# Performance work log

Measured on AMD Instinct MI355X. Metric: run time of the kernel, lower is better.

## Reference

```python
import jax, jax.numpy as jnp
import numpy as np

N_NODES = 50000
N_EDGES = 500000
D = 256  # node_dim = edge_dim = out_dim; in_dim = 2*D


def setup_inputs() -> dict:
    key = jax.random.key(0)
    ks = jax.random.split(key, 9)
    x = jax.random.normal(ks[0], (N_NODES, D), dtype=jnp.float32)
    edge_index = jax.random.randint(ks[1], (2, N_EDGES), 0, N_NODES, dtype=jnp.int64)
    edge_attr = jax.random.normal(ks[2], (N_EDGES, D), dtype=jnp.float32)
    u = jax.random.normal(ks[3], (1, D), dtype=jnp.float32)
    batch = jnp.zeros((N_NODES,), dtype=jnp.int64)
    scale = 1.0 / np.sqrt(2 * D)
    W1 = jax.random.normal(ks[4], (2 * D, D), dtype=jnp.float32) * scale
    b1 = jax.random.normal(ks[5], (D,), dtype=jnp.float32) * scale
    W2 = jax.random.normal(ks[6], (2 * D, D), dtype=jnp.float32) * scale
    b2 = jax.random.normal(ks[7], (D,), dtype=jnp.float32) * scale
    return {"x": x, "edge_index": edge_index, "edge_attr": edge_attr, "u": u,
            "batch": batch, "W1": W1, "b1": b1, "W2": W2, "b2": b2}


def reference(x, edge_index, edge_attr, u, batch, W1, b1, W2, b2):
    row, col = edge_index[0], edge_index[1]
    # gather source-node features and concat with edge features: [E, 2D]
    h = jnp.concatenate([x[row], edge_attr], axis=1)
    h = jax.nn.relu(h @ W1 + b1)  # node_mlp_1
    # scatter-mean over destination nodes
    agg = jax.ops.segment_sum(h, col, num_segments=N_NODES)
    cnt = jax.ops.segment_sum(jnp.ones((h.shape[0],), h.dtype), col, num_segments=N_NODES)
    agg = agg / jnp.maximum(cnt, 1.0)[:, None]
    out = jnp.concatenate([x, agg], axis=1)  # [N, 2D]
    return jax.nn.relu(out @ W2 + b2)  # node_mlp_2
```

## Files before the change

### kernel.cpp

```cpp
#include <hip/hip_runtime.h>

#define N_NODES 50000
#define N_EDGES 500000
#define D 256
#define TWO_D 512

typedef __attribute__((ext_vector_type(8))) __bf16 bf16x8;
typedef __attribute__((ext_vector_type(4))) float f32x4;
typedef unsigned short ushort_t;

__device__ __forceinline__ unsigned short f2bf(float f) {
    unsigned int u = __builtin_bit_cast(unsigned int, f);
    u += 0x7FFFu + ((u >> 16) & 1u);
    return (unsigned short)(u >> 16);
}
__device__ __forceinline__ unsigned int pk2(float lo, float hi) {
    return (unsigned int)f2bf(lo) | ((unsigned int)f2bf(hi) << 16);
}
__device__ __forceinline__ float bf2f(ushort_t u) {
    return __builtin_bit_cast(float, ((unsigned int)u) << 16);
}


__global__ void k_zero(float* __restrict__ p, int n4) {
    int i = blockIdx.x * blockDim.x + threadIdx.x;
    if (i < n4) ((float4*)p)[i] = make_float4(0.f, 0.f, 0.f, 0.f);
}

__global__ void k_cvt_x(const float* __restrict__ x, ushort_t* __restrict__ xb, int n8) {
    int i = blockIdx.x * blockDim.x + threadIdx.x;
    if (i < n8) {
        const float4* s = (const float4*)(x + (size_t)i * 8);
        float4 a = s[0], b = s[1];
        uint4 o;
        o.x = pk2(a.x, a.y); o.y = pk2(a.z, a.w);
        o.z = pk2(b.x, b.y); o.w = pk2(b.z, b.w);
        *(uint4*)(xb + (size_t)i * 8) = o;
    }
}

__global__ void k_wt(const float* __restrict__ w, ushort_t* __restrict__ wt) {
    int n = blockIdx.x;
    for (int k = threadIdx.x; k < TWO_D; k += blockDim.x)
        wt[(size_t)n * TWO_D + k] = f2bf(w[(size_t)k * D + n]);
}

__global__ void k_count_i(const int* __restrict__ coli, int* __restrict__ cnt) {
    int e = blockIdx.x * blockDim.x + threadIdx.x;
    if (e < N_EDGES) atomicAdd(&cnt[coli[e]], 1);
}

__global__ void k_count_f(const int* __restrict__ coli, float* __restrict__ cnt) {
    int e = blockIdx.x * blockDim.x + threadIdx.x;
    if (e < N_EDGES) atomicAdd(&cnt[coli[e]], 1.0f);
}


__device__ __forceinline__ int iscan_block(int v, int tid) {
    int lane = tid & 63, wv = tid >> 6;
    int s = v;
    #pragma unroll
    for (int off = 1; off < 64; off <<= 1) {
        int t = __shfl_up(s, off, 64);
        if (lane >= off) s += t;
    }
    __shared__ int wsum[4];
    if (lane == 63) wsum[wv] = s;
    __syncthreads();
    #pragma unroll
    for (int w = 0; w < 3; ++w)
        if (wv > w) s += wsum[w];
    return s;
}

__global__ void k_scan_a(const int* __restrict__ cnt, int* __restrict__ rowptr,
                         int* __restrict__ bsum) {
    int i = blockIdx.x * 256 + threadIdx.x;
    int v = (i < N_NODES) ? cnt[i] : 0;
    int s = iscan_block(v, threadIdx.x);
    if (i < N_NODES) rowptr[i] = s - v;
    if (threadIdx.x == 255) bsum[blockIdx.x] = s;
}

__global__ void k_scan_b(int* __restrict__ bsum, int nb) {
    int i = threadIdx.x;
    int v = (i < nb) ? bsum[i] : 0;
    int s = iscan_block(v, i);
    if (i < nb) bsum[i] = s - v;
}

__global__ void k_scan_c(int* __restrict__ rowptr, const int* __restrict__ bsum,
                         int* __restrict__ cursor) {
    int i = blockIdx.x * 256 + threadIdx.x;
    if (i < N_NODES) {
        int r = rowptr[i] + bsum[blockIdx.x];
        rowptr[i] = r;
        cursor[i] = r;
    }
    if (i == 0) rowptr[N_NODES] = N_EDGES;
}

__global__ void k_fill(const int* __restrict__ coli, int* __restrict__ cursor,
                       int* __restrict__ elist) {
    int e = blockIdx.x * blockDim.x + threadIdx.x;
    if (e < N_EDGES) {
        int p = atomicAdd(&cursor[coli[e]], 1);
        elist[p] = e;
    }
}

template<bool CSR>
__global__ __launch_bounds__(256) void k_edge_t(
    const ushort_t* __restrict__ xb, const float* __restrict__ ea,
    const ushort_t* __restrict__ w1t, const float* __restrict__ b1,
    const int* __restrict__ rowi, const int* __restrict__ coli,
    ushort_t* __restrict__ h, float* __restrict__ agg)
{
    __shared__ __align__(16) ushort_t As[64 * 64];
    __shared__ __align__(16) ushort_t Bs[256 * 64];
    const int tid = threadIdx.x;
    const int wave = tid >> 6, lane = tid & 63;
    const int lr = lane & 15, lh = lane >> 4;
    const int e0 = blockIdx.x * 64;

    const int sm = tid >> 2;
    const int sc = (tid & 3) << 4;
    int es = e0 + sm; if (es >= N_EDGES) es = N_EDGES - 1;
    const int srow = rowi[es];
    const ushort_t* xrow  = xb + (size_t)srow * D;
    const float*    earow = ea + (size_t)es * D;
    const ushort_t* wrow  = w1t + (size_t)tid * TWO_D;
    const int swA = (sm & 7) << 3;
    const int swB = (tid & 7) << 3;

    f32x4 acc[4][4];
    #pragma unroll
    for (int i = 0; i < 4; ++i)
        #pragma unroll
        for (int j = 0; j < 4; ++j)
            acc[i][j] = (f32x4){0.f, 0.f, 0.f, 0.f};

    for (int kk = 0; kk < 8; ++kk) {
        const int k0 = kk << 6;
        uint4 av0, av1;
        if (kk < 4) {
            const uint4* s = (const uint4*)(xrow + k0 + sc);
            av0 = s[0]; av1 = s[1];
        } else {
            const float4* s = (const float4*)(earow + (k0 - D) + sc);
            float4 f0 = s[0], f1 = s[1], f2 = s[2], f3 = s[3];
            av0.x = pk2(f0.x, f0.y); av0.y = pk2(f0.z, f0.w);
            av0.z = pk2(f1.x, f1.y); av0.w = pk2(f1.z, f1.w);
            av1.x = pk2(f2.x, f2.y); av1.y = pk2(f2.z, f2.w);
            av1.z = pk2(f3.x, f3.y); av1.w = pk2(f3.z, f3.w);
        }
        const uint4* wsv = (const uint4*)(wrow + k0);
        uint4 w0 = wsv[0], w1 = wsv[1], w2 = wsv[2], w3 = wsv[3];
        uint4 w4 = wsv[4], w5 = wsv[5], w6 = wsv[6], w7 = wsv[7];

        __syncthreads();
        *(uint4*)&As[sm * 64 + ( sc      ^ swA)] = av0;
        *(uint4*)&As[sm * 64 + ((sc + 8) ^ swA)] = av1;
        {
            const int base = tid * 64;
            *(uint4*)&Bs[base + ( 0 ^ swB)] = w0;
            *(uint4*)&Bs[base + ( 8 ^ swB)] = w1;
            *(uint4*)&Bs[base + (16 ^ swB)] = w2;
            *(uint4*)&Bs[base + (24 ^ swB)] = w3;
            *(uint4*)&Bs[base + (32 ^ swB)] = w4;
            *(uint4*)&Bs[base + (40 ^ swB)] = w5;
            *(uint4*)&Bs[base + (48 ^ swB)] = w6;
            *(uint4*)&Bs[base + (56 ^ swB)] = w7;
        }
        __syncthreads();

        #pragma unroll
        for (int kh = 0; kh < 2; ++kh) {
            const int kb = kh * 32 + lh * 8;
            bf16x8 af[4], bfr[4];
            #pragma unroll
            for (int i = 0; i < 4; ++i) {
                int m = i * 16 + lr;
                af[i] = *(const bf16x8*)&As[m * 64 + (kb ^ ((m & 7) << 3))];
            }
            #pragma unroll
            for (int j = 0; j < 4; ++j) {
                int n = wave * 64 + j * 16 + lr;
                bfr[j] = *(const bf16x8*)&Bs[n * 64 + (kb ^ ((n & 7) << 3))];
            }
            #pragma unroll
            for (int i = 0; i < 4; ++i)
                #pragma unroll
                for (int j = 0; j < 4; ++j)
                    acc[i][j] = __builtin_amdgcn_mfma_f32_16x16x32_bf16(af[i], bfr[j], acc[i][j], 0, 0, 0);
        }
    }

    float bv[4];
    #pragma unroll
    for (int j = 0; j < 4; ++j) bv[j] = b1[wave * 64 + j * 16 + lr];
    #pragma unroll
    for (int i = 0; i < 4; ++i) {
        #pragma unroll
        for (int r = 0; r < 4; ++r) {
            int m = i * 16 + lh * 4 + r;
            int e = e0 + m;
            if (e < N_EDGES) {
                if constexpr (CSR) {
                    ushort_t* hrow = h + (size_t)e * D + wave * 64 + lr;
                    #pragma unroll
                    for (int j = 0; j < 4; ++j) {
                        float v = acc[i][j][r] + bv[j];
                        hrow[j * 16] = f2bf(v > 0.f ? v : 0.f);
                    }
                } else {
                    float* arow = agg + (size_t)coli[e] * D;
                    #pragma unroll
                    for (int j = 0; j < 4; ++j) {
                        float v = acc[i][j][r] + bv[j];
                        if (v > 0.f) atomicAdd(&arow[wave * 64 + j * 16 + lr], v);
                    }
                }
            }
        }
    }
}

__global__ __launch_bounds__(256) void k_agg(
    const ushort_t* __restrict__ h, const int* __restrict__ rowptr,
    const int* __restrict__ elist, ushort_t* __restrict__ aggb)
{
    int node = blockIdx.x * 4 + (threadIdx.x >> 6);
    if (node >= N_NODES) return;
    int lane = threadIdx.x & 63;
    int beg = rowptr[node], end = rowptr[node + 1];
    float a0 = 0.f, a1 = 0.f, a2 = 0.f, a3 = 0.f;
    int p = beg;
    int e_nxt = (p < end) ? elist[p] : 0;
    while (p < end) {
        int e = e_nxt;
        if (p + 1 < end) e_nxt = elist[p + 1];
        ushort4 u = *(const ushort4*)(h + (size_t)e * D + lane * 4);
        a0 += bf2f(u.x); a1 += bf2f(u.y); a2 += bf2f(u.z); a3 += bf2f(u.w);
        ++p;
    }
    float inv = 1.0f / fmaxf((float)(end - beg), 1.0f);
    ushort4 o;
    o.x = f2bf(a0 * inv); o.y = f2bf(a1 * inv);
    o.z = f2bf(a2 * inv); o.w = f2bf(a3 * inv);
    *(ushort4*)(aggb + (size_t)node * D + lane * 4) = o;
}

template<bool CSR>
__global__ __launch_bounds__(256) void k_node_t(
    const ushort_t* __restrict__ xb, const ushort_t* __restrict__ aggb,
    const float* __restrict__ aggf, const float* __restrict__ cnt,
    const ushort_t* __restrict__ w2t, const float* __restrict__ b2,
    float* __restrict__ out)
{
    __shared__ __align__(16) ushort_t As[64 * 64];
    __shared__ __align__(16) ushort_t Bs[256 * 64];
    const int tid = threadIdx.x;
    const int wave = tid >> 6, lane = tid & 63;
    const int lr = lane & 15, lh = lane >> 4;
    const int n0 = blockIdx.x * 64;

    const int sm = tid >> 2;
    const int sc = (tid & 3) << 4;
    int ns = n0 + sm; if (ns >= N_NODES) ns = N_NODES - 1;
    const ushort_t* xrow = xb + (size_t)ns * D;
    const ushort_t* abrow = CSR ? (aggb + (size_t)ns * D) : nullptr;
    const float*    afrow = CSR ? nullptr : (aggf + (size_t)ns * D);
    const float     ic    = CSR ? 1.0f : (1.0f / fmaxf(cnt[ns], 1.0f));
    const ushort_t* wrow = w2t + (size_t)tid * TWO_D;
    const int swA = (sm & 7) << 3;
    const int swB = (tid & 7) << 3;

    f32x4 acc[4][4];
    #pragma unroll
    for (int i = 0; i < 4; ++i)
        #pragma unroll
        for (int j = 0; j < 4; ++j)
            acc[i][j] = (f32x4){0.f, 0.f, 0.f, 0.f};

    for (int kk = 0; kk < 8; ++kk) {
        const int k0 = kk << 6;
        uint4 av0, av1;
        if (kk < 4) {
            const uint4* s = (const uint4*)(xrow + k0 + sc);
            av0 = s[0]; av1 = s[1];
        } else if constexpr (CSR) {
            const uint4* s = (const uint4*)(abrow + (k0 - D) + sc);
            av0 = s[0]; av1 = s[1];
        } else {
            const float4* s = (const float4*)(afrow + (k0 - D) + sc);
            float4 f0 = s[0], f1 = s[1], f2 = s[2], f3 = s[3];
            f0.x *= ic; f0.y *= ic; f0.z *= ic; f0.w *= ic;
            f1.x *= ic; f1.y *= ic; f1.z *= ic; f1.w *= ic;
            f2.x *= ic; f2.y *= ic; f2.z *= ic; f2.w *= ic;
            f3.x *= ic; f3.y *= ic; f3.z *= ic; f3.w *= ic;
            av0.x = pk2(f0.x, f0.y); av0.y = pk2(f0.z, f0.w);
            av0.z = pk2(f1.x, f1.y); av0.w = pk2(f1.z, f1.w);
            av1.x = pk2(f2.x, f2.y); av1.y = pk2(f2.z, f2.w);
            av1.z = pk2(f3.x, f3.y); av1.w = pk2(f3.z, f3.w);
        }
        const uint4* wsv = (const uint4*)(wrow + k0);
        uint4 w0 = wsv[0], w1 = wsv[1], w2 = wsv[2], w3 = wsv[3];
        uint4 w4 = wsv[4], w5 = wsv[5], w6 = wsv[6], w7 = wsv[7];

        __syncthreads();
        *(uint4*)&As[sm * 64 + ( sc      ^ swA)] = av0;
        *(uint4*)&As[sm * 64 + ((sc + 8) ^ swA)] = av1;
        {
            const int base = tid * 64;
            *(uint4*)&Bs[base + ( 0 ^ swB)] = w0;
            *(uint4*)&Bs[base + ( 8 ^ swB)] = w1;
            *(uint4*)&Bs[base + (16 ^ swB)] = w2;
            *(uint4*)&Bs[base + (24 ^ swB)] = w3;
            *(uint4*)&Bs[base + (32 ^ swB)] = w4;
            *(uint4*)&Bs[base + (40 ^ swB)] = w5;
            *(uint4*)&Bs[base + (48 ^ swB)] = w6;
            *(uint4*)&Bs[base + (56 ^ swB)] = w7;
        }
        __syncthreads();

        #pragma unroll
        for (int kh = 0; kh < 2; ++kh) {
            const int kb = kh * 32 + lh * 8;
            bf16x8 af[4], bfr[4];
            #pragma unroll
            for (int i = 0; i < 4; ++i) {
                int m = i * 16 + lr;
                af[i] = *(const bf16x8*)&As[m * 64 + (kb ^ ((m & 7) << 3))];
            }
            #pragma unroll
            for (int j = 0; j < 4; ++j) {
                int n = wave * 64 + j * 16 + lr;
                bfr[j] = *(const bf16x8*)&Bs[n * 64 + (kb ^ ((n & 7) << 3))];
            }
            #pragma unroll
            for (int i = 0; i < 4; ++i)
                #pragma unroll
                for (int j = 0; j < 4; ++j)
                    acc[i][j] = __builtin_amdgcn_mfma_f32_16x16x32_bf16(af[i], bfr[j], acc[i][j], 0, 0, 0);
        }
    }

    float bv[4];
    #pragma unroll
    for (int j = 0; j < 4; ++j) bv[j] = b2[wave * 64 + j * 16 + lr];
    #pragma unroll
    for (int i = 0; i < 4; ++i) {
        #pragma unroll
        for (int r = 0; r < 4; ++r) {
            int m = i * 16 + lh * 4 + r;
            int node = n0 + m;
            if (node < N_NODES) {
                float* orow = out + (size_t)node * D;
                #pragma unroll
                for (int j = 0; j < 4; ++j) {
                    float v = acc[i][j][r] + bv[j];
                    orow[wave * 64 + j * 16 + lr] = v > 0.f ? v : 0.f;
                }
            }
        }
    }
}


extern "C" void kernel_launch(void* const* d_in, const int* in_sizes, int n_in,
                              void* d_out, int out_size, void* d_ws, size_t ws_size,
                              hipStream_t stream)
{
    const float* x  = (const float*)d_in[0];
    const int*   ei = (const int*)d_in[1];
    const float* ea = (const float*)d_in[2];
    const float* W1 = (const float*)d_in[5];
    const float* b1 = (const float*)d_in[6];
    const float* W2 = (const float*)d_in[7];
    const float* b2 = (const float*)d_in[8];
    float* out = (float*)d_out;

    const int* rowi = ei;
    const int* coli = ei + N_EDGES;
    char* ws = (char*)d_ws;

    size_t off = 0;
    auto take = [&](size_t bytes) {
        char* p = ws + off;
        off = (off + bytes + 255) & ~(size_t)255;
        return p;
    };

    ushort_t* xb  = (ushort_t*)take((size_t)N_NODES * D * 2);
    ushort_t* w1t = (ushort_t*)take((size_t)D * TWO_D * 2);
    ushort_t* w2t = (ushort_t*)take((size_t)D * TWO_D * 2);
    size_t off_common = off;

    ushort_t* aggb   = (ushort_t*)take((size_t)N_NODES * D * 2);
    ushort_t* h      = (ushort_t*)take((size_t)N_EDGES * D * 2);
    int*      cnti   = (int*)take(50016 * 4);
    int*      rowptr = (int*)take(50016 * 4);
    int*      cursor = (int*)take(50016 * 4);
    int*      bsum   = (int*)take(256 * 4);
    int*      elist  = (int*)take((size_t)N_EDGES * 4);
    const bool use_csr = (off <= ws_size);

    k_cvt_x<<<(N_NODES * D / 8 + 255) / 256, 256, 0, stream>>>(x, xb, N_NODES * D / 8);
    k_wt   <<<D, 256, 0, stream>>>(W1, w1t);
    k_wt   <<<D, 256, 0, stream>>>(W2, w2t);

    if (use_csr) {
        const int NB = (N_NODES + 255) / 256;
        k_zero   <<<49, 256, 0, stream>>>((float*)cnti, 50016 / 4);
        k_count_i<<<(N_EDGES + 255) / 256, 256, 0, stream>>>(coli, cnti);
        k_scan_a <<<NB, 256, 0, stream>>>(cnti, rowptr, bsum);
        k_scan_b <<<1, 256, 0, stream>>>(bsum, NB);
        k_scan_c <<<NB, 256, 0, stream>>>(rowptr, bsum, cursor);
        k_fill   <<<(N_EDGES + 255) / 256, 256, 0, stream>>>(coli, cursor, elist);
        k_edge_t<true><<<(N_EDGES + 63) / 64, 256, 0, stream>>>(
            xb, ea, w1t, b1, rowi, coli, h, nullptr);
        k_agg    <<<(N_NODES + 3) / 4, 256, 0, stream>>>(h, rowptr, elist, aggb);
        k_node_t<true><<<(N_NODES + 63) / 64, 256, 0, stream>>>(
            xb, aggb, nullptr, nullptr, w2t, b2, out);
    } else {
        off = off_common;
        float* aggf = (float*)take((size_t)(N_NODES * D + 50048) * 4);
        float* cntf = aggf + (size_t)N_NODES * D;
        const int zf4 = (N_NODES * D + 50048) / 4;
        k_zero   <<<(zf4 + 255) / 256, 256, 0, stream>>>(aggf, zf4);
        k_count_f<<<(N_EDGES + 255) / 256, 256, 0, stream>>>(coli, cntf);
        k_edge_t<false><<<(N_EDGES + 63) / 64, 256, 0, stream>>>(
            xb, ea, w1t, b1, rowi, coli, nullptr, aggf);
        k_node_t<false><<<(N_NODES + 63) / 64, 256, 0, stream>>>(
            xb, nullptr, aggf, cntf, w2t, b2, out);
    }
}
```

Baseline: 555.0 us.

## Split W1 into node and edge halves, fuse segmented aggregation into edge GEMM

Splits the first MLP into a per-node product x·W1a (computed once for 50k nodes) and a per-edge product edge_attr·W1b. This halves the edge GEMM's K dimension and removes the per-edge gather of x rows. Edges are processed in CSR-sorted order, and each block does an in-shared-memory segmented sum by destination node. It writes a sum directly when a node's segment lies entirely inside the block and falls back to atomics otherwise, which removes the bf16 h buffer and the separate aggregation kernel. In exchange it adds an fp32 xw1 buffer that is gathered per edge, reads edge_attr in scattered order through elist, and adds a binary-search posnode kernel plus zeroing of an fp32 agg array.

Result: slower. 795.5 us (+43.3%).

```diff
diff --git a/kernel.cpp b/kernel.cpp
--- a/kernel.cpp
+++ b/kernel.cpp
@@ -39,20 +39,15 @@
     }
 }
 
-__global__ void k_wt(const float* __restrict__ w, ushort_t* __restrict__ wt) {
+__global__ void k_wt(const float* __restrict__ w, ushort_t* __restrict__ wt, int KW) {
     int n = blockIdx.x;
-    for (int k = threadIdx.x; k < TWO_D; k += blockDim.x)
-        wt[(size_t)n * TWO_D + k] = f2bf(w[(size_t)k * D + n]);
+    for (int k = threadIdx.x; k < KW; k += blockDim.x)
+        wt[(size_t)n * KW + k] = f2bf(w[(size_t)k * D + n]);
 }
 
 __global__ void k_count_i(const int* __restrict__ coli, int* __restrict__ cnt) {
     int e = blockIdx.x * blockDim.x + threadIdx.x;
     if (e < N_EDGES) atomicAdd(&cnt[coli[e]], 1);
-}
-
-__global__ void k_count_f(const int* __restrict__ coli, float* __restrict__ cnt) {
-    int e = blockIdx.x * blockDim.x + threadIdx.x;
-    if (e < N_EDGES) atomicAdd(&cnt[coli[e]], 1.0f);
 }
 
 
@@ -100,36 +95,44 @@
     if (i == 0) rowptr[N_NODES] = N_EDGES;
 }
 
-__global__ void k_fill(const int* __restrict__ coli, int* __restrict__ cursor,
-                       int* __restrict__ elist) {
+__global__ void k_fill(const int* __restrict__ coli, const int* __restrict__ rowi,
+                       int* __restrict__ cursor, int* __restrict__ elist,
+                       int* __restrict__ rowg) {
     int e = blockIdx.x * blockDim.x + threadIdx.x;
     if (e < N_EDGES) {
         int p = atomicAdd(&cursor[coli[e]], 1);
         elist[p] = e;
-    }
-}
-
-template<bool CSR>
-__global__ __launch_bounds__(256) void k_edge_t(
-    const ushort_t* __restrict__ xb, const float* __restrict__ ea,
-    const ushort_t* __restrict__ w1t, const float* __restrict__ b1,
-    const int* __restrict__ rowi, const int* __restrict__ coli,
-    ushort_t* __restrict__ h, float* __restrict__ agg)
+        rowg[p] = rowi[e];
+    }
+}
+
+__global__ void k_posnode(const int* __restrict__ rowptr, int* __restrict__ posnode) {
+    int p = blockIdx.x * blockDim.x + threadIdx.x;
+    if (p >= N_EDGES) return;
+    int lo = 0, hi = N_NODES;
+    while (hi - lo > 1) {
+        int mid = (lo + hi) >> 1;
+        if (rowptr[mid] <= p) lo = mid; else hi = mid;
+    }
+    posnode[p] = lo;
+}
+
+__global__ __launch_bounds__(256) void k_xw1(
+    const ushort_t* __restrict__ xb, const ushort_t* __restrict__ w1at,
+    const float* __restrict__ b1, float* __restrict__ xw1)
 {
     __shared__ __align__(16) ushort_t As[64 * 64];
     __shared__ __align__(16) ushort_t Bs[256 * 64];
     const int tid = threadIdx.x;
     const int wave = tid >> 6, lane = tid & 63;
     const int lr = lane & 15, lh = lane >> 4;
-    const int e0 = blockIdx.x * 64;
+    const int n0 = blockIdx.x * 64;
 
     const int sm = tid >> 2;
     const int sc = (tid & 3) << 4;
-    int es = e0 + sm; if (es >= N_EDGES) es = N_EDGES - 1;
-    const int srow = rowi[es];
-    const ushort_t* xrow  = xb + (size_t)srow * D;
-    const float*    earow = ea + (size_t)es * D;
-    const ushort_t* wrow  = w1t + (size_t)tid * TWO_D;
+    int ns = n0 + sm; if (ns >= N_NODES) ns = N_NODES - 1;
+    const ushort_t* xrow = xb + (size_t)ns * D;
+    const ushort_t* wrow = w1at + (size_t)tid * D;
     const int swA = (sm & 7) << 3;
     const int swB = (tid & 7) << 3;
 
@@ -140,20 +143,10 @@
         for (int j = 0; j < 4; ++j)
             acc[i][j] = (f32x4){0.f, 0.f, 0.f, 0.f};
 
-    for (int kk = 0; kk < 8; ++kk) {
+    for (int kk = 0; kk < 4; ++kk) {
         const int k0 = kk << 6;
-        uint4 av0, av1;
-        if (kk < 4) {
-            const uint4* s = (const uint4*)(xrow + k0 + sc);
-            av0 = s[0]; av1 = s[1];
-        } else {
-            const float4* s = (const float4*)(earow + (k0 - D) + sc);
-            float4 f0 = s[0], f1 = s[1], f2 = s[2], f3 = s[3];
-            av0.x = pk2(f0.x, f0.y); av0.y = pk2(f0.z, f0.w);
-            av0.z = pk2(f1.x, f1.y); av0.w = pk2(f1.z, f1.w);
-            av1.x = pk2(f2.x, f2.y); av1.y = pk2(f2.z, f2.w);
-            av1.z = pk2(f3.x, f3.y); av1.w = pk2(f3.z, f3.w);
-        }
+        const uint4* sx = (const uint4*)(xrow + k0 + sc);
+        uint4 av0 = sx[0], av1 = sx[1];
         const uint4* wsv = (const uint4*)(wrow + k0);
         uint4 w0 = wsv[0], w1 = wsv[1], w2 = wsv[2], w3 = wsv[3];
         uint4 w4 = wsv[4], w5 = wsv[5], w6 = wsv[6], w7 = wsv[7];
@@ -204,75 +197,36 @@
         #pragma unroll
         for (int r = 0; r < 4; ++r) {
             int m = i * 16 + lh * 4 + r;
-            int e = e0 + m;
-            if (e < N_EDGES) {
-                if constexpr (CSR) {
-                    ushort_t* hrow = h + (size_t)e * D + wave * 64 + lr;
-                    #pragma unroll
-                    for (int j = 0; j < 4; ++j) {
-                        float v = acc[i][j][r] + bv[j];
-                        hrow[j * 16] = f2bf(v > 0.f ? v : 0.f);
-                    }
-                } else {
-                    float* arow = agg + (size_t)coli[e] * D;
-                    #pragma unroll
-                    for (int j = 0; j < 4; ++j) {
-                        float v = acc[i][j][r] + bv[j];
-                        if (v > 0.f) atomicAdd(&arow[wave * 64 + j * 16 + lr], v);
-                    }
-                }
-            }
-        }
-    }
-}
-
-__global__ __launch_bounds__(256) void k_agg(
-    const ushort_t* __restrict__ h, const int* __restrict__ rowptr,
-    const int* __restrict__ elist, ushort_t* __restrict__ aggb)
-{
-    int node = blockIdx.x * 4 + (threadIdx.x >> 6);
-    if (node >= N_NODES) return;
-    int lane = threadIdx.x & 63;
-    int beg = rowptr[node], end = rowptr[node + 1];
-    float a0 = 0.f, a1 = 0.f, a2 = 0.f, a3 = 0.f;
-    int p = beg;
-    int e_nxt = (p < end) ? elist[p] : 0;
-    while (p < end) {
-        int e = e_nxt;
-        if (p + 1 < end) e_nxt = elist[p + 1];
-        ushort4 u = *(const ushort4*)(h + (size_t)e * D + lane * 4);
-        a0 += bf2f(u.x); a1 += bf2f(u.y); a2 += bf2f(u.z); a3 += bf2f(u.w);
-        ++p;
-    }
-    float inv = 1.0f / fmaxf((float)(end - beg), 1.0f);
-    ushort4 o;
-    o.x = f2bf(a0 * inv); o.y = f2bf(a1 * inv);
-    o.z = f2bf(a2 * inv); o.w = f2bf(a3 * inv);
-    *(ushort4*)(aggb + (size_t)node * D + lane * 4) = o;
-}
-
-template<bool CSR>
-__global__ __launch_bounds__(256) void k_node_t(
-    const ushort_t* __restrict__ xb, const ushort_t* __restrict__ aggb,
-    const float* __restrict__ aggf, const float* __restrict__ cnt,
-    const ushort_t* __restrict__ w2t, const float* __restrict__ b2,
-    float* __restrict__ out)
+            int node = n0 + m;
+            if (node < N_NODES) {
+                float* orow = xw1 + (size_t)node * D;
+                #pragma unroll
+                for (int j = 0; j < 4; ++j)
+                    orow[wave * 64 + j * 16 + lr] = acc[i][j][r] + bv[j];
+            }
+        }
+    }
+}
+
+__global__ __launch_bounds__(256) void k_edge_csr(
+    const float* __restrict__ ea, const ushort_t* __restrict__ w1bt,
+    const float* __restrict__ xw1, const int* __restrict__ elist,
+    const int* __restrict__ rowg, const int* __restrict__ posnode,
+    const int* __restrict__ rowptr, float* __restrict__ agg)
 {
     __shared__ __align__(16) ushort_t As[64 * 64];
     __shared__ __align__(16) ushort_t Bs[256 * 64];
     const int tid = threadIdx.x;
     const int wave = tid >> 6, lane = tid & 63;
     const int lr = lane & 15, lh = lane >> 4;
-    const int n0 = blockIdx.x * 64;
+    const int p0 = blockIdx.x * 64;
 
     const int sm = tid >> 2;
     const int sc = (tid & 3) << 4;
-    int ns = n0 + sm; if (ns >= N_NODES) ns = N_NODES - 1;
-    const ushort_t* xrow = xb + (size_t)ns * D;
-    const ushort_t* abrow = CSR ? (aggb + (size_t)ns * D) : nullptr;
-    const float*    afrow = CSR ? nullptr : (aggf + (size_t)ns * D);
-    const float     ic    = CSR ? 1.0f : (1.0f / fmaxf(cnt[ns], 1.0f));
-    const ushort_t* wrow = w2t + (size_t)tid * TWO_D;
+    int ps = p0 + sm; if (ps >= N_EDGES) ps = N_EDGES - 1;
+    const int es = elist[ps];
+    const float* earow = ea + (size_t)es * D;
+    const ushort_t* wrow = w1bt + (size_t)tid * D;
     const int swA = (sm & 7) << 3;
     const int swB = (tid & 7) << 3;
 
@@ -283,27 +237,16 @@
         for (int j = 0; j < 4; ++j)
             acc[i][j] = (f32x4){0.f, 0.f, 0.f, 0.f};
 
-    for (int kk = 0; kk < 8; ++kk) {
+    #pragma unroll 1
+    for (int kk = 0; kk < 4; ++kk) {
         const int k0 = kk << 6;
+        const float4* s = (const float4*)(earow + k0 + sc);
+        float4 f0 = s[0], f1 = s[1], f2 = s[2], f3 = s[3];
         uint4 av0, av1;
-        if (kk < 4) {
-            const uint4* s = (const uint4*)(xrow + k0 + sc);
-            av0 = s[0]; av1 = s[1];
-        } else if constexpr (CSR) {
-            const uint4* s = (const uint4*)(abrow + (k0 - D) + sc);
-            av0 = s[0]; av1 = s[1];
-        } else {
-            const float4* s = (const float4*)(afrow + (k0 - D) + sc);
-            float4 f0 = s[0], f1 = s[1], f2 = s[2], f3 = s[3];
-            f0.x *= ic; f0.y *= ic; f0.z *= ic; f0.w *= ic;
-            f1.x *= ic; f1.y *= ic; f1.z *= ic; f1.w *= ic;
-            f2.x *= ic; f2.y *= ic; f2.z *= ic; f2.w *= ic;
-            f3.x *= ic; f3.y *= ic; f3.z *= ic; f3.w *= ic;
-            av0.x = pk2(f0.x, f0.y); av0.y = pk2(f0.z, f0.w);
-            av0.z = pk2(f1.x, f1.y); av0.w = pk2(f1.z, f1.w);
-            av1.x = pk2(f2.x, f2.y); av1.y = pk2(f2.z, f2.w);
-            av1.z = pk2(f3.x, f3.y); av1.w = pk2(f3.z, f3.w);
-        }
+        av0.x = pk2(f0.x, f0.y); av0.y = pk2(f0.z, f0.w);
+        av0.z = pk2(f1.x, f1.y); av0.w = pk2(f1.z, f1.w);
+        av1.x = pk2(f2.x, f2.y); av1.y = pk2(f2.z, f2.w);
+        av1.z = pk2(f3.x, f3.y); av1.w = pk2(f3.z, f3.w);
         const uint4* wsv = (const uint4*)(wrow + k0);
         uint4 w0 = wsv[0], w1 = wsv[1], w2 = wsv[2], w3 = wsv[3];
         uint4 w4 = wsv[4], w5 = wsv[5], w6 = wsv[6], w7 = wsv[7];
@@ -346,6 +289,152 @@
         }
     }
 
+    __syncthreads();
+    int* snd = (int*)As;
+    if (tid < 64) snd[tid] = posnode[min(p0 + tid, N_EDGES - 1)];
+
+    #pragma unroll
+    for (int i = 0; i < 4; ++i) {
+        #pragma unroll
+        for (int r = 0; r < 4; ++r) {
+            const int m = i * 16 + lh * 4 + r;
+            const int p = p0 + m;
+            const bool ok = (p < N_EDGES);
+            const int srow = ok ? rowg[p] : 0;
+            const float* xr = xw1 + (size_t)srow * D + wave * 64 + lr;
+            #pragma unroll
+            for (int j = 0; j < 4; ++j) {
+                float v = ok ? (acc[i][j][r] + xr[j * 16]) : 0.f;
+                v = v > 0.f ? v : 0.f;
+                const int n = wave * 64 + j * 16 + lr;
+                Bs[m * 256 + (n ^ (((m >> 2) & 3) << 2))] = f2bf(v);
+            }
+        }
+    }
+    __syncthreads();
+
+    const int c = tid;
+    int node = snd[0];
+    float s = 0.f;
+    #pragma unroll 1
+    for (int rr = 0; rr < 64; rr += 8) {
+        float v[8];
+        int nd[8];
+        #pragma unroll
+        for (int q = 0; q < 8; ++q) {
+            int r = rr + q;
+            v[q] = bf2f(Bs[r * 256 + (c ^ (((r >> 2) & 3) << 2))]);
+            nd[q] = snd[r];
+        }
+        #pragma unroll
+        for (int q = 0; q < 8; ++q) {
+            if (nd[q] != node) {
+                float* dst = agg + (size_t)node * D + c;
+                if (rowptr[node] >= p0 && rowptr[node + 1] <= p0 + 64) *dst = s;
+                else atomicAdd(dst, s);
+                node = nd[q];
+                s = 0.f;
+            }
+            s += v[q];
+        }
+    }
+    {
+        float* dst = agg + (size_t)node * D + c;
+        if (rowptr[node] >= p0 && rowptr[node + 1] <= p0 + 64) *dst = s;
+        else atomicAdd(dst, s);
+    }
+}
+
+__global__ __launch_bounds__(256) void k_node(
+    const ushort_t* __restrict__ xb, const float* __restrict__ agg,
+    const int* __restrict__ cnti,
+    const ushort_t* __restrict__ w2t, const float* __restrict__ b2,
+    float* __restrict__ out)
+{
+    __shared__ __align__(16) ushort_t As[64 * 64];
+    __shared__ __align__(16) ushort_t Bs[256 * 64];
+    const int tid = threadIdx.x;
+    const int wave = tid >> 6, lane = tid & 63;
+    const int lr = lane & 15, lh = lane >> 4;
+    const int n0 = blockIdx.x * 64;
+
+    const int sm = tid >> 2;
+    const int sc = (tid & 3) << 4;
+    int ns = n0 + sm; if (ns >= N_NODES) ns = N_NODES - 1;
+    const ushort_t* xrow = xb + (size_t)ns * D;
+    const float*    arow = agg + (size_t)ns * D;
+    const float     ic   = 1.0f / fmaxf((float)cnti[ns], 1.0f);
+    const ushort_t* wrow = w2t + (size_t)tid * TWO_D;
+    const int swA = (sm & 7) << 3;
+    const int swB = (tid & 7) << 3;
+
+    f32x4 acc[4][4];
+    #pragma unroll
+    for (int i = 0; i < 4; ++i)
+        #pragma unroll
+        for (int j = 0; j < 4; ++j)
+            acc[i][j] = (f32x4){0.f, 0.f, 0.f, 0.f};
+
+    for (int kk = 0; kk < 8; ++kk) {
+        const int k0 = kk << 6;
+        uint4 av0, av1;
+        if (kk < 4) {
+            const uint4* s = (const uint4*)(xrow + k0 + sc);
+            av0 = s[0]; av1 = s[1];
+        } else {
+            const float4* s = (const float4*)(arow + (k0 - D) + sc);
+            float4 f0 = s[0], f1 = s[1], f2 = s[2], f3 = s[3];
+            f0.x *= ic; f0.y *= ic; f0.z *= ic; f0.w *= ic;
+            f1.x *= ic; f1.y *= ic; f1.z *= ic; f1.w *= ic;
+            f2.x *= ic; f2.y *= ic; f2.z *= ic; f2.w *= ic;
+            f3.x *= ic; f3.y *= ic; f3.z *= ic; f3.w *= ic;
+            av0.x = pk2(f0.x, f0.y); av0.y = pk2(f0.z, f0.w);
+            av0.z = pk2(f1.x, f1.y); av0.w = pk2(f1.z, f1.w);
+            av1.x = pk2(f2.x, f2.y); av1.y = pk2(f2.z, f2.w);
+            av1.z = pk2(f3.x, f3.y); av1.w = pk2(f3.z, f3.w);
+        }
+        const uint4* wsv = (const uint4*)(wrow + k0);
+        uint4 w0 = wsv[0], w1 = wsv[1], w2 = wsv[2], w3 = wsv[3];
+        uint4 w4 = wsv[4], w5 = wsv[5], w6 = wsv[6], w7 = wsv[7];
+
+        __syncthreads();
+        *(uint4*)&As[sm * 64 + ( sc      ^ swA)] = av0;
+        *(uint4*)&As[sm * 64 + ((sc + 8) ^ swA)] = av1;
+        {
+            const int base = tid * 64;
+            *(uint4*)&Bs[base + ( 0 ^ swB)] = w0;
+            *(uint4*)&Bs[base + ( 8 ^ swB)] = w1;
+            *(uint4*)&Bs[base + (16 ^ swB)] = w2;
+            *(uint4*)&Bs[base + (24 ^ swB)] = w3;
+            *(uint4*)&Bs[base + (32 ^ swB)] = w4;
+            *(uint4*)&Bs[base + (40 ^ swB)] = w5;
+            *(uint4*)&Bs[base + (48 ^ swB)] = w6;
+            *(uint4*)&Bs[base + (56 ^ swB)] = w7;
+        }
+        __syncthreads();
+
+        #pragma unroll
+        for (int kh = 0; kh < 2; ++kh) {
+            const int kb = kh * 32 + lh * 8;
+            bf16x8 af[4], bfr[4];
+            #pragma unroll
+            for (int i = 0; i < 4; ++i) {
+                int m = i * 16 + lr;
+                af[i] = *(const bf16x8*)&As[m * 64 + (kb ^ ((m & 7) << 3))];
+            }
+            #pragma unroll
+            for (int j = 0; j < 4; ++j) {
+                int n = wave * 64 + j * 16 + lr;
+                bfr[j] = *(const bf16x8*)&Bs[n * 64 + (kb ^ ((n & 7) << 3))];
+            }
+            #pragma unroll
+            for (int i = 0; i < 4; ++i)
+                #pragma unroll
+                for (int j = 0; j < 4; ++j)
+                    acc[i][j] = __builtin_amdgcn_mfma_f32_16x16x32_bf16(af[i], bfr[j], acc[i][j], 0, 0, 0);
+        }
+    }
+
     float bv[4];
     #pragma unroll
     for (int j = 0; j < 4; ++j) bv[j] = b2[wave * 64 + j * 16 + lr];
@@ -392,47 +481,40 @@
         return p;
     };
 
-    ushort_t* xb  = (ushort_t*)take((size_t)N_NODES * D * 2);
-    ushort_t* w1t = (ushort_t*)take((size_t)D * TWO_D * 2);
-    ushort_t* w2t = (ushort_t*)take((size_t)D * TWO_D * 2);
-    size_t off_common = off;
-
-    ushort_t* aggb   = (ushort_t*)take((size_t)N_NODES * D * 2);
-    ushort_t* h      = (ushort_t*)take((size_t)N_EDGES * D * 2);
-    int*      cnti   = (int*)take(50016 * 4);
-    int*      rowptr = (int*)take(50016 * 4);
-    int*      cursor = (int*)take(50016 * 4);
-    int*      bsum   = (int*)take(256 * 4);
-    int*      elist  = (int*)take((size_t)N_EDGES * 4);
-    const bool use_csr = (off <= ws_size);
+    ushort_t* xb      = (ushort_t*)take((size_t)N_NODES * D * 2);
+    ushort_t* w1at    = (ushort_t*)take((size_t)D * D * 2);
+    ushort_t* w1bt    = (ushort_t*)take((size_t)D * D * 2);
+    ushort_t* w2t     = (ushort_t*)take((size_t)D * TWO_D * 2);
+    float*    xw1     = (float*)take((size_t)N_NODES * D * 4);
+    float*    agg     = (float*)take((size_t)N_NODES * D * 4);
+    int*      cnti    = (int*)take(50016 * 4);
+    int*      rowptr  = (int*)take(50016 * 4);
+    int*      cursor  = (int*)take(50016 * 4);
+    int*      bsum    = (int*)take(256 * 4);
+    int*      elist   = (int*)take((size_t)N_EDGES * 4);
+    int*      rowg    = (int*)take((size_t)N_EDGES * 4);
+    int*      posnode = (int*)take((size_t)N_EDGES * 4);
+
+    const int NB = (N_NODES + 255) / 256;
+    const int EB = (N_EDGES + 255) / 256;
+    const int NGB = (N_NODES + 63) / 64;
+    const int EGB = (N_EDGES + 63) / 64;
 
     k_cvt_x<<<(N_NODES * D / 8 + 255) / 256, 256, 0, stream>>>(x, xb, N_NODES * D / 8);
-    k_wt   <<<D, 256, 0, stream>>>(W1, w1t);
-    k_wt   <<<D, 256, 0, stream>>>(W2, w2t);
-
-    if (use_csr) {
-        const int NB = (N_NODES + 255) / 256;
-        k_zero   <<<49, 256, 0, stream>>>((float*)cnti, 50016 / 4);
-        k_count_i<<<(N_EDGES + 255) / 256, 256, 0, stream>>>(coli, cnti);
-        k_scan_a <<<NB, 256, 0, stream>>>(cnti, rowptr, bsum);
-        k_scan_b <<<1, 256, 0, stream>>>(bsum, NB);
-        k_scan_c <<<NB, 256, 0, stream>>>(rowptr, bsum, cursor);
-        k_fill   <<<(N_EDGES + 255) / 256, 256, 0, stream>>>(coli, cursor, elist);
-        k_edge_t<true><<<(N_EDGES + 63) / 64, 256, 0, stream>>>(
-            xb, ea, w1t, b1, rowi, coli, h, nullptr);
-        k_agg    <<<(N_NODES + 3) / 4, 256, 0, stream>>>(h, rowptr, elist, aggb);
-        k_node_t<true><<<(N_NODES + 63) / 64, 256, 0, stream>>>(
-            xb, aggb, nullptr, nullptr, w2t, b2, out);
-    } else {
-        off = off_common;
-        float* aggf = (float*)take((size_t)(N_NODES * D + 50048) * 4);
-        float* cntf = aggf + (size_t)N_NODES * D;
-        const int zf4 = (N_NODES * D + 50048) / 4;
-        k_zero   <<<(zf4 + 255) / 256, 256, 0, stream>>>(aggf, zf4);
-        k_count_f<<<(N_EDGES + 255) / 256, 256, 0, stream>>>(coli, cntf);
-        k_edge_t<false><<<(N_EDGES + 63) / 64, 256, 0, stream>>>(
-            xb, ea, w1t, b1, rowi, coli, nullptr, aggf);
-        k_node_t<false><<<(N_NODES + 63) / 64, 256, 0, stream>>>(
-            xb, nullptr, aggf, cntf, w2t, b2, out);
-    }
-}
+    k_wt   <<<D, 256, 0, stream>>>(W1, w1at, D);
+    k_wt   <<<D, 256, 0, stream>>>(W1 + (size_t)D * D, w1bt, D);
+    k_wt   <<<D, 256, 0, stream>>>(W2, w2t, TWO_D);
+
+    k_zero   <<<49, 256, 0, stream>>>((float*)cnti, 50016 / 4);
+    k_count_i<<<EB, 256, 0, stream>>>(coli, cnti);
+    k_scan_a <<<NB, 256, 0, stream>>>(cnti, rowptr, bsum);
+    k_scan_b <<<1, 256, 0, stream>>>(bsum, NB);
+    k_scan_c <<<NB, 256, 0, stream>>>(rowptr, bsum, cursor);
+    k_fill   <<<EB, 256, 0, stream>>>(coli, rowi, cursor, elist, rowg);
+    k_posnode<<<EB, 256, 0, stream>>>(rowptr, posnode);
+
+    k_xw1    <<<NGB, 256, 0, stream>>>(xb, w1at, b1, xw1);
+    k_zero   <<<(N_NODES * D / 4 + 255) / 256, 256, 0, stream>>>(agg, N_NODES * D / 4);
+    k_edge_csr<<<EGB, 256, 0, stream>>>(ea, w1bt, xw1, elist, rowg, posnode, rowptr, agg);
+    k_node   <<<NGB, 256, 0, stream>>>(xb, agg, cnti, w2t, b2, out);
+}
```
